# Performance work log

Measured on AMD Instinct MI355X. Metric: run time of the kernel, lower is better.

Reference implementation:

```python
import jax, jax.numpy as jnp
import numpy as np


def _conv2d(x, w, b=None):
    # 3x3, stride 1, pad 1, NCHW
    out = jax.lax.conv_general_dilated(x, w, (1, 1), ((1, 1), (1, 1)),
                                       dimension_numbers=('NCHW', 'OIHW', 'NCHW'))
    return out if b is None else out + b[None, :, None, None]


def _bn(x, g, beta, m, v, eps=1e-5):
    # inference-mode BatchNorm2d with running stats
    inv = g / jnp.sqrt(v + eps)
    return x * inv[None, :, None, None] + (beta - m * inv)[None, :, None, None]


def _se(x, w1, w2):
    # SELayer: global avgpool -> FC(C->C/r) -> ReLU -> FC(C/r->C) -> sigmoid -> scale
    s = x.mean((2, 3))                       # [B,C]
    s = jax.nn.sigmoid(jax.nn.relu(s @ w1.T) @ w2.T)
    return x * s[:, :, None, None]


def _bilinear(x, py, px):
    # zero-padded bilinear sampling; x [B,C,H,W], py/px [B,K,H,W] -> [B,C,K,H,W]
    B, C, H, W = x.shape
    K = py.shape[1]
    xf = x.reshape(B, C, H * W)
    y0 = jnp.floor(py)
    x0 = jnp.floor(px)
    out = jnp.zeros((B, C, K, H, W), x.dtype)
    for oy, ox in ((0., 0.), (0., 1.), (1., 0.), (1., 1.)):
        yc = y0 + oy
        xc = x0 + ox
        wgt = (1. - jnp.abs(py - yc)) * (1. - jnp.abs(px - xc))
        valid = ((yc >= 0) & (yc < H) & (xc >= 0) & (xc < W)).astype(x.dtype)
        idx = (jnp.clip(yc, 0, H - 1) * W + jnp.clip(xc, 0, W - 1)).astype(jnp.int32)
        g = jnp.take_along_axis(xf, idx.reshape(B, 1, -1), axis=2).reshape(B, C, K, H, W)
        out = out + g * (wgt * valid)[:, None]
    return out


def _dcnv2(x, w_off, b_off, w, b):
    # ModulatedDeformConv2dPack: conv_offset -> (o1,o2,mask); interleaved (dy,dx) pairs
    B, C, H, W = x.shape
    K = 9  # 3x3 kernel
    off = _conv2d(x, w_off, b_off)            # [B,27,H,W]
    o = off[:, :2 * K]
    mask = jax.nn.sigmoid(off[:, 2 * K:])     # [B,9,H,W]
    dy = o[:, 0::2]
    dx = o[:, 1::2]
    ky = (jnp.arange(K) // 3 - 1).astype(x.dtype)
    kx = (jnp.arange(K) % 3 - 1).astype(x.dtype)
    py = dy + jnp.arange(H, dtype=x.dtype)[None, None, :, None] + ky[None, :, None, None]
    px = dx + jnp.arange(W, dtype=x.dtype)[None, None, None, :] + kx[None, :, None, None]
    s = _bilinear(x, py, px) * mask[:, None]  # [B,C,9,H,W]
    return jnp.einsum('bckhw,ock->bohw', s, w.reshape(w.shape[0], C, K)) + b[None, :, None, None]


def _sfe(x, y, se_w1, se_w2, off_w, off_b, enc_w, enc_b,
         we_w, we_b, we_g, we_beta, we_m, we_v,
         wf_w, wf_b, wf_g, wf_beta, wf_m, wf_v):
    base = x + y
    base = base + _se(base, se_w1, se_w2)
    enc = jax.nn.relu(_dcnv2(base, off_w, off_b, enc_w, enc_b))
    w_e = jax.nn.sigmoid(_bn(_conv2d(enc, we_w, we_b), we_g, we_beta, we_m, we_v))
    w_f = jax.nn.sigmoid(_bn(_conv2d(enc, wf_w, wf_b), wf_g, wf_beta, wf_m, wf_v))
    return w_e * x + w_f * y


def setup_inputs() -> dict:
    B, C, CC, H, W = 4, 256, 64, 64, 64
    R = 16  # SE reduction
    key = jax.random.key(0)
    ks = jax.random.split(key, 12)
    f = jnp.float32
    return {
        'x': jax.random.normal(ks[0], (B, C, H, W), f),
        'y': jax.random.normal(ks[1], (B, C, H, W), f),
        'se_w1': jax.random.normal(ks[2], (C // R, C), f) * 0.05,
        'se_w2': jax.random.normal(ks[3], (C, C // R), f) * 0.05,
        'off_w': jax.random.normal(ks[4], (27, C, 3, 3), f) * 0.01,
        'off_b': jnp.zeros((27,), f),
        'enc_w': jax.random.normal(ks[5], (CC, C, 3, 3), f) * 0.02,
        'enc_b': jnp.zeros((CC,), f),
        'we_w': jax.random.normal(ks[6], (C, CC, 3, 3), f) * 0.02,
        'we_b': jnp.zeros((C,), f),
        'we_g': jnp.ones((C,), f),
        'we_beta': jnp.zeros((C,), f),
        'we_m': jax.random.normal(ks[7], (C,), f) * 0.01,
        'we_v': jnp.ones((C,), f),
        'wf_w': jax.random.normal(ks[8], (C, CC, 3, 3), f) * 0.02,
        'wf_b': jnp.zeros((C,), f),
        'wf_g': jnp.ones((C,), f),
        'wf_beta': jnp.zeros((C,), f),
        'wf_m': jax.random.normal(ks[9], (C,), f) * 0.01,
        'wf_v': jnp.ones((C,), f),
    }


def reference(x, y, se_w1, se_w2, off_w, off_b, enc_w, enc_b,
              we_w, we_b, we_g, we_beta, we_m, we_v,
              wf_w, wf_b, wf_g, wf_beta, wf_m, wf_v):
    return _sfe(x, y, se_w1, se_w2, off_w, off_b, enc_w, enc_b,
                we_w, we_b, we_g, we_beta, we_m, we_v,
                wf_w, wf_b, wf_g, wf_beta, wf_m, wf_v)
```

## Files before the change

### kernel.cpp

```cpp
#include <hip/hip_runtime.h>
#include <math.h>

#define BB 4
#define CH 256
#define CCH 64
#define HH 64
#define WW 64
#define HWN 4096

typedef short s8v __attribute__((ext_vector_type(8)));
typedef float f4v __attribute__((ext_vector_type(4)));

__device__ __forceinline__ float sigmoidf_(float v){ return 1.0f/(1.0f+__expf(-v)); }
__device__ __forceinline__ unsigned short f2bf(float f){
    union{float f; unsigned u;} v; v.f=f;
    unsigned r = v.u + 0x7FFF + ((v.u>>16)&1);
    return (unsigned short)(r>>16);
}
__device__ __forceinline__ float bf2f(unsigned short u){
    union{unsigned u; float f;} v; v.u = ((unsigned)u)<<16; return v.f;
}

__global__ __launch_bounds__(256) void k_prepall(const float* __restrict__ enc_w,
    const float* __restrict__ wew, const float* __restrict__ wfw, const float* __restrict__ ow,
    const float* __restrict__ web, const float* __restrict__ weg, const float* __restrict__ webt,
    const float* __restrict__ wem, const float* __restrict__ wev,
    const float* __restrict__ wfb, const float* __restrict__ wfg, const float* __restrict__ wfbt,
    const float* __restrict__ wfm, const float* __restrict__ wfv,
    unsigned short* __restrict__ wdcn, unsigned short* __restrict__ w2,
    unsigned short* __restrict__ wofft, float* __restrict__ bnp){
    int i = blockIdx.x*256+threadIdx.x;
    if (i < 147456){
        int oc = i/2304, kk = i-oc*2304;
        int k = kk>>8, c = kk&255;
        wdcn[i] = f2bf(enc_w[(size_t)oc*2304 + c*9 + k]);
        return;
    }
    int j = i - 147456;
    if (j < 294912){
        int row = j/576, k = j-row*576;
        int t = k>>6, ic = k&63;
        float v = (row<256)? wew[((row<<6)+ic)*9+t] : wfw[(((row-256)<<6)+ic)*9+t];
        w2[j] = f2bf(v);
        return;
    }
    int m = j - 294912;
    if (m < 73728){
        int ko = m/2304, k = m-ko*2304;
        int t = k>>8, c = k&255;
        wofft[m] = f2bf((ko<27)? ow[(size_t)(ko*256+c)*9+t] : 0.f);
        return;
    }
    int n = m - 73728;
    if (n < 256){
        float ie = weg[n]*rsqrtf(wev[n]+1e-5f);
        float se = webt[n]-wem[n]*ie+web[n]*ie;
        float iff = wfg[n]*rsqrtf(wfv[n]+1e-5f);
        float sf = wfbt[n]-wfm[n]*iff+wfb[n]*iff;
        *(float4*)(bnp+n*4) = make_float4(ie,se,iff,sf);
    }
}

__global__ __launch_bounds__(256) void k_base_sum(const float* __restrict__ x, const float* __restrict__ y,
                                                  float* __restrict__ base, float* __restrict__ sums){
    int bc = blockIdx.x, tid = threadIdx.x;
    const float* xp = x + (size_t)bc*HWN;
    const float* yp = y + (size_t)bc*HWN;
    float* bp = base + (size_t)bc*HWN;
    float s = 0.f;
    for (int i=tid;i<HWN;i+=256){ float v = xp[i]+yp[i]; bp[i]=v; s+=v; }
    __shared__ float red[256];
    red[tid]=s; __syncthreads();
    for (int off=128; off>0; off>>=1){ if (tid<off) red[tid]+=red[tid+off]; __syncthreads(); }
    if (tid==0) sums[bc]=red[0];
}

__global__ __launch_bounds__(256) void k_se(const float* __restrict__ sums, const float* __restrict__ w1,
                                            const float* __restrict__ w2, float* __restrict__ scale){
    int b = blockIdx.x, tid = threadIdx.x;
    __shared__ float sm[256];
    __shared__ float hid[16];
    sm[tid] = sums[b*256+tid]*(1.0f/4096.0f);
    __syncthreads();
    if (tid<16){
        float a=0.f; const float* wp = w1 + tid*256;
        for (int c=0;c<256;c++) a += sm[c]*wp[c];
        hid[tid]=fmaxf(a,0.f);
    }
    __syncthreads();
    float a=0.f; const float* wp = w2 + tid*16;
    #pragma unroll
    for (int j=0;j<16;j++) a += hid[j]*wp[j];
    scale[b*256+tid] = 1.f + sigmoidf_(a);
}

__global__ __launch_bounds__(256) void k_scale_t(const float* __restrict__ base, const float* __restrict__ scale,
                                                 unsigned short* __restrict__ base_t){
    int bid = blockIdx.x;
    int pb = bid&63, cb = (bid>>6)&3, b = bid>>8;
    int tid = threadIdx.x;
    __shared__ unsigned short lt[64*66];
    #pragma unroll
    for (int it=0; it<16; ++it){
        int idx = it*256 + tid;
        int c = idx>>6, p = idx&63;
        size_t gi = ((size_t)(b*256 + cb*64 + c))*4096 + pb*64 + p;
        float v = base[gi] * scale[b*256 + cb*64 + c];
        lt[p*66 + c] = f2bf(v);
    }
    __syncthreads();
    #pragma unroll
    for (int it=0; it<8; ++it){
        int idx = it*256 + tid;
        int p = idx>>5, cp = idx&31;
        unsigned lo = lt[p*66 + cp*2], hi = lt[p*66 + cp*2+1];
        *(unsigned*)(base_t + ((size_t)(b*4096 + pb*64 + p))*256 + cb*64 + cp*2) = lo | (hi<<16);
    }
}

__global__ __launch_bounds__(512) void k_offconv_mfma(const unsigned short* __restrict__ base_t,
    const unsigned short* __restrict__ wofft, const float* __restrict__ ob, float* __restrict__ off){
    int bid = blockIdx.x;
    int tIdx = bid&63, b = bid>>6;
    int th = tIdx>>3, tw = tIdx&7;
    int tid = threadIdx.x;
    __shared__ unsigned short plds[3200*8];
    const unsigned short* bt = base_t + (((size_t)b)<<12)*256;
    for (int i=tid; i<3200; i+=512){
        int spot = i>>5, cid = i&31;
        int sy = spot/10, sx = spot - sy*10;
        int gy = th*8 + sy - 1, gx = tw*8 + sx - 1;
        uint4 v = make_uint4(0u,0u,0u,0u);
        if (gy>=0 && gy<HH && gx>=0 && gx<WW)
            v = *(const uint4*)(bt + ((size_t)((gy<<6)+gx))*256 + cid*8);
        int chunk = (spot<<5) | (cid ^ (spot&7));
        *(uint4*)(plds + (chunk<<3)) = v;
    }
    __syncthreads();
    int lane = tid&63, w = tid>>6;
    int rf = w&1, pf = w>>1;
    int col = lane&15, kg = lane>>4;
    int p = pf*16 + col, ly = p>>3, lx = p&7;
    f4v acc = (f4v){0.f,0.f,0.f,0.f};
    #pragma unroll
    for (int j=0;j<9;j++){
        int dy = j/3, dx = j%3;
        int spot = (ly+dy)*10 + lx+dx;
        const unsigned short* arow = wofft + (size_t)(rf*16+col)*2304 + j*256 + kg*8;
        #pragma unroll
        for (int s=0;s<8;s++){
            s8v a = *(const s8v*)(arow + s*32);
            int cid = s*4 + kg;
            s8v bf = *(const s8v*)(plds + (((spot<<5)|(cid^(spot&7)))<<3));
            acc = __builtin_amdgcn_mfma_f32_16x16x32_bf16(a, bf, acc, 0,0,0);
        }
    }
    int gy = th*8+ly, gx = tw*8+lx;
    #pragma unroll
    for (int r=0;r<4;r++){
        int ko = rf*16 + kg*4 + r;
        if (ko < 27)
            off[(((size_t)(b*27+ko))<<12) + (gy<<6) + gx] = acc[r] + ob[ko];
    }
}

__global__ __launch_bounds__(256) void k_prep_off(const float* __restrict__ off,
                                                  float4* __restrict__ cwg, int4* __restrict__ cig){
    int i = blockIdx.x*256+threadIdx.x;
    if (i >= 147456) return;
    int b = i/36864, rem = i - b*36864;
    int k = rem>>12, pos = rem&4095;
    int h = pos>>6, p = pos&63;
    const float* op = off + ((size_t)b*27<<12) + pos;
    float dy = op[(size_t)(2*k)<<12];
    float dx = op[(size_t)(2*k+1)<<12];
    float m  = sigmoidf_(op[(size_t)(18+k)<<12]);
    float py = (float)(h + k/3 - 1) + dy;
    float px = (float)(p + (k%3) - 1) + dx;
    float y0 = floorf(py), x0 = floorf(px);
    float fy1 = py - y0, fy0 = 1.f - fy1;
    float fx1 = px - x0, fx0 = 1.f - fx1;
    int iy0 = (int)y0, ix0 = (int)x0;
    bool vy0 = (y0>=0.f)&&(y0<64.f), vy1 = (y0>=-1.f)&&(y0<63.f);
    bool vx0 = (x0>=0.f)&&(x0<64.f), vx1 = (x0>=-1.f)&&(x0<63.f);
    int cy0 = min(max(iy0,0),63), cy1 = min(max(iy0+1,0),63);
    int cx0 = min(max(ix0,0),63), cx1 = min(max(ix0+1,0),63);
    float4 wv; int4 iv;
    wv.x = (vy0&&vx0)? fy0*fx0*m : 0.f;
    wv.y = (vy0&&vx1)? fy0*fx1*m : 0.f;
    wv.z = (vy1&&vx0)? fy1*fx0*m : 0.f;
    wv.w = (vy1&&vx1)? fy1*fx1*m : 0.f;
    iv.x = cy0*WW+cx0; iv.y = cy0*WW+cx1; iv.z = cy1*WW+cx0; iv.w = cy1*WW+cx1;
    cwg[i] = wv; cig[i] = iv;
}

__global__ __launch_bounds__(512) void k_dcn_mfma(const unsigned short* __restrict__ base_t,
    const float4* __restrict__ cwg, const int4* __restrict__ cig,
    const unsigned short* __restrict__ wdcn, unsigned short* __restrict__ part2b){
    int bid = blockIdx.x;
    int cg = bid&3, b = (bid>>2)&3, h = bid>>4;
    int tid = threadIdx.x;
    __shared__ float4 cw4[576];
    __shared__ int4   ci4[576];
    __shared__ unsigned short smp[2][4096];

    for (int i=tid;i<576;i+=512){
        int k = i>>6, p = i&63;
        size_t g = (((size_t)b*9 + k)<<12) + (h<<6) + p;
        cw4[i] = cwg[g];
        ci4[i] = cig[g];
    }
    __syncthreads();

    int pos = tid>>3, cv = tid&7;
    int w = tid>>6, lane = tid&63;
    int mf = w&3, nh = w>>2;
    int col = lane&15, kg = lane>>4;
    f4v acc0 = (f4v){0.f,0.f,0.f,0.f}, acc1 = acc0;
    const unsigned short* bt = base_t + (((size_t)b)<<12)*256 + cg*64 + cv*8;
    const unsigned short* wrow = wdcn + (size_t)(mf*16+col)*2304 + cg*64;

    #pragma unroll
    for (int t=0;t<9;t++){
        float4 wv = cw4[t*64+pos];
        int4  iv = ci4[t*64+pos];
        uint4 r0 = *(const uint4*)(bt + ((size_t)iv.x<<8));
        uint4 r1 = *(const uint4*)(bt + ((size_t)iv.y<<8));
        uint4 r2 = *(const uint4*)(bt + ((size_t)iv.z<<8));
        uint4 r3 = *(const uint4*)(bt + ((size_t)iv.w<<8));
        const unsigned* q0=(const unsigned*)&r0;
        const unsigned* q1=(const unsigned*)&r1;
        const unsigned* q2=(const unsigned*)&r2;
        const unsigned* q3=(const unsigned*)&r3;
        unsigned pk[4];
        #pragma unroll
        for (int d=0;d<4;d++){
            float lo = wv.x*bf2f((unsigned short)(q0[d]&0xFFFFu)) + wv.y*bf2f((unsigned short)(q1[d]&0xFFFFu))
                     + wv.z*bf2f((unsigned short)(q2[d]&0xFFFFu)) + wv.w*bf2f((unsigned short)(q3[d]&0xFFFFu));
            float hi = wv.x*bf2f((unsigned short)(q0[d]>>16)) + wv.y*bf2f((unsigned short)(q1[d]>>16))
                     + wv.z*bf2f((unsigned short)(q2[d]>>16)) + wv.w*bf2f((unsigned short)(q3[d]>>16));
            pk[d] = (unsigned)f2bf(lo) | ((unsigned)f2bf(hi)<<16);
        }
        *(uint4*)(&smp[t&1][0] + (((pos<<3)|(cv^(pos&7)))<<3)) = *(const uint4*)pk;
        __syncthreads();
        const unsigned short* sb = &smp[t&1][0];
        #pragma unroll
        for (int ks=0;ks<2;ks++){
            s8v a = *(const s8v*)(wrow + t*256 + ks*32 + kg*8);
            int cgrp = ks*4+kg;
            int p0 = (nh*2)*16 + col;
            int p1 = p0 + 16;
            s8v b0 = *(const s8v*)(sb + (((p0<<3)|(cgrp^(p0&7)))<<3));
            s8v b1 = *(const s8v*)(sb + (((p1<<3)|(cgrp^(p1&7)))<<3));
            acc0 = __builtin_amdgcn_mfma_f32_16x16x32_bf16(a, b0, acc0, 0,0,0);
            acc1 = __builtin_amdgcn_mfma_f32_16x16x32_bf16(a, b1, acc1, 0,0,0);
        }
    }

    unsigned short* pout = part2b + ((size_t)(cg*BB + b))*(HWN*64);
    #pragma unroll
    for (int j=0;j<2;j++){
        f4v a = j ? acc1 : acc0;
        int posg = (h<<6) + (nh*2+j)*16 + col;
        int oc = mf*16 + kg*4;
        unsigned lo = (unsigned)f2bf(a[0]) | ((unsigned)f2bf(a[1])<<16);
        unsigned hi = (unsigned)f2bf(a[2]) | ((unsigned)f2bf(a[3])<<16);
        *(uint2*)(pout + (size_t)posg*64 + oc) = make_uint2(lo,hi);
    }
}

__global__ __launch_bounds__(256) void k_encreduce(const unsigned short* __restrict__ part2b,
                                                   const float* __restrict__ encb,
                                                   unsigned short* __restrict__ enc_t){
    int i = blockIdx.x*256+threadIdx.x;
    int b = i>>17, rem = i&131071;
    int pos = rem>>5, oc2 = rem&31;
    size_t basei = (((size_t)b<<12) + pos)*64 + oc2*2;
    float s0 = encb[oc2*2], s1 = encb[oc2*2+1];
    #pragma unroll
    for (int cg=0;cg<4;cg++){
        unsigned pv = *(const unsigned*)(part2b + (size_t)cg*1048576 + basei);
        s0 += bf2f((unsigned short)(pv & 0xFFFFu));
        s1 += bf2f((unsigned short)(pv >> 16));
    }
    unsigned short lo = f2bf(fmaxf(s0,0.f));
    unsigned short hi = f2bf(fmaxf(s1,0.f));
    *(unsigned int*)(enc_t + basei) = (unsigned int)lo | ((unsigned int)hi<<16);
}

__global__ __launch_bounds__(512) void k_fuse_mfma(const unsigned short* __restrict__ enc_t,
    const unsigned short* __restrict__ w2, const float* __restrict__ bnp,
    const float* __restrict__ x, const float* __restrict__ y, float* __restrict__ out){
    int bid = blockIdx.x;
    int ocg = bid&3, tile = (bid>>2)&15, b = bid>>6;
    int h0 = (tile>>2)<<4, w0 = (tile&3)<<4;
    int tid = threadIdx.x;
    __shared__ unsigned short elds[324*64];

    const unsigned short* ebase = enc_t + (((size_t)b)<<12)*64;
    #pragma unroll
    for (int kk=0;kk<6;kk++){
        int i = tid + kk*512;
        if (i < 2592){
            int sp = i>>3, icg = i&7;
            int sy = sp/18, sx = sp - sy*18;
            int py = h0+sy-1, px = w0+sx-1;
            uint4 v = make_uint4(0u,0u,0u,0u);
            if (py>=0 && py<HH && px>=0 && px<WW)
                v = *(const uint4*)(ebase + (size_t)((py<<6)+px)*64 + (icg<<3));
            int chunk = ((sp<<3) | icg) ^ (sp&7);
            *(uint4*)(elds + (chunk<<3)) = v;
        }
    }
    __syncthreads();

    int lane = tid&63, w = tid>>6;
    int col = lane&15, kg = lane>>4;
    f4v acc[8][2];
    #pragma unroll
    for (int rf=0;rf<8;rf++)
        #pragma unroll
        for (int pf=0;pf<2;pf++) acc[rf][pf] = (f4v){0.f,0.f,0.f,0.f};

    #pragma unroll
    for (int t=0;t<18;t++){
        const int j = t>>1, ih = t&1;
        const int dy = j/3-1, dx = j%3-1;
        s8v af[8];
        #pragma unroll
        for (int rf=0;rf<8;rf++){
            int row = (rf<4 ? ocg*64 + rf*16 : 256 + ocg*64 + (rf-4)*16) + col;
            af[rf] = *(const s8v*)(w2 + (size_t)row*576 + t*32 + kg*8);
        }
        s8v bfr[2];
        #pragma unroll
        for (int pf=0;pf<2;pf++){
            int tyc = w*2+pf;
            int sp = (tyc+dy+1)*18 + (col+dx+1);
            int chunk = ((sp<<3) | (ih*4+kg)) ^ (sp&7);
            bfr[pf] = *(const s8v*)(elds + (chunk<<3));
        }
        #pragma unroll
        for (int rf=0;rf<8;rf++)
            #pragma unroll
            for (int pf=0;pf<2;pf++)
                acc[rf][pf] = __builtin_amdgcn_mfma_f32_16x16x32_bf16(af[rf], bfr[pf], acc[rf][pf], 0,0,0);
    }

    #pragma unroll
    for (int rf=0;rf<4;rf++){
        #pragma unroll
        for (int pf=0;pf<2;pf++){
            int tyc = w*2+pf;
            int py = h0+tyc, px = w0+col;
            #pragma unroll
            for (int r=0;r<4;r++){
                int oc = ocg*64 + rf*16 + kg*4 + r;
                float4 bn = *(const float4*)(bnp + oc*4);
                float ve = sigmoidf_(acc[rf  ][pf][r]*bn.x + bn.y);
                float vf = sigmoidf_(acc[rf+4][pf][r]*bn.z + bn.w);
                size_t oi = (((size_t)((b<<8)+oc))<<12) + (py<<6) + px;
                out[oi] = ve*x[oi] + vf*y[oi];
            }
        }
    }
}

extern "C" void kernel_launch(void* const* d_in, const int* in_sizes, int n_in,
                              void* d_out, int out_size, void* d_ws, size_t ws_size,
                              hipStream_t stream) {
    const float* x     = (const float*)d_in[0];
    const float* y     = (const float*)d_in[1];
    const float* se_w1 = (const float*)d_in[2];
    const float* se_w2 = (const float*)d_in[3];
    const float* off_w = (const float*)d_in[4];
    const float* off_b = (const float*)d_in[5];
    const float* enc_w = (const float*)d_in[6];
    const float* enc_b = (const float*)d_in[7];
    const float* we_w  = (const float*)d_in[8];
    const float* we_b  = (const float*)d_in[9];
    const float* we_g  = (const float*)d_in[10];
    const float* we_bt = (const float*)d_in[11];
    const float* we_m  = (const float*)d_in[12];
    const float* we_v  = (const float*)d_in[13];
    const float* wf_w  = (const float*)d_in[14];
    const float* wf_b  = (const float*)d_in[15];
    const float* wf_g  = (const float*)d_in[16];
    const float* wf_bt = (const float*)d_in[17];
    const float* wf_m  = (const float*)d_in[18];
    const float* wf_v  = (const float*)d_in[19];
    float* out = (float*)d_out;

    float* ws     = (float*)d_ws;
    float* base   = ws;
    float* off    = base + 4194304;
    float* encT_f = off  + 442368;
    float* sums   = encT_f + 524288;
    float* scale  = sums + 1024;
    float* wdcn_f = scale + 1024;
    float* w2f    = wdcn_f + 73728;
    float* bnp    = w2f  + 147456;
    float* wofft_f= bnp  + 1024;
    float* cw_f   = wofft_f + 36864;
    float* ci_f   = cw_f + 589824;
    unsigned short* enc_t = (unsigned short*)encT_f;
    unsigned short* wdcn  = (unsigned short*)wdcn_f;
    unsigned short* w2    = (unsigned short*)w2f;
    unsigned short* wofft = (unsigned short*)wofft_f;
    float4* cwg = (float4*)cw_f;
    int4*   cig = (int4*)ci_f;
    unsigned short* base_t = (unsigned short*)out;
    unsigned short* part2b = (unsigned short*)out + 4194304;

    k_prepall     <<<2018, 256, 0, stream>>>(enc_w, we_w, wf_w, off_w,
                                             we_b, we_g, we_bt, we_m, we_v,
                                             wf_b, wf_g, wf_bt, wf_m, wf_v,
                                             wdcn, w2, wofft, bnp);
    k_base_sum    <<<1024, 256, 0, stream>>>(x, y, base, sums);
    k_se          <<<4,    256, 0, stream>>>(sums, se_w1, se_w2, scale);
    k_scale_t     <<<1024, 256, 0, stream>>>(base, scale, base_t);
    k_offconv_mfma<<<256,  512, 0, stream>>>(base_t, wofft, off_b, off);
    k_prep_off    <<<576,  256, 0, stream>>>(off, cwg, cig);
    k_dcn_mfma    <<<1024, 512, 0, stream>>>(base_t, cwg, cig, wdcn, part2b);
    k_encreduce   <<<2048, 256, 0, stream>>>(part2b, enc_b, enc_t);
    k_fuse_mfma   <<<256,  512, 0, stream>>>(enc_t, w2, bnp, x, y, out);
}
```

Before: 240.6 us.

## Fold SE channel scale into per-batch conv weights and fuse base transpose

The SE per-channel scale is now folded into per-batch bf16 copies of the DCN and offset-conv weights, so the activation no longer needs a scale pass. The x+y sum, channel sums (via wave shuffles and atomics) and the bf16 transpose are merged into a single kernel, removing the fp32 base buffer round trip. The fuse kernel also doubles its block count, with half the output channels per block, to raise parallelism. In exchange, weights are replicated per batch, a memset and atomic adds are added, and rounding shifts because the scale is applied to weights instead of activations.

```diff
diff --git a/kernel.cpp b/kernel.cpp
--- a/kernel.cpp
+++ b/kernel.cpp
@@ -21,37 +21,22 @@
     union{unsigned u; float f;} v; v.u = ((unsigned)u)<<16; return v.f;
 }
 
-__global__ __launch_bounds__(256) void k_prepall(const float* __restrict__ enc_w,
-    const float* __restrict__ wew, const float* __restrict__ wfw, const float* __restrict__ ow,
+__global__ __launch_bounds__(256) void k_prepall(
+    const float* __restrict__ wew, const float* __restrict__ wfw,
     const float* __restrict__ web, const float* __restrict__ weg, const float* __restrict__ webt,
     const float* __restrict__ wem, const float* __restrict__ wev,
     const float* __restrict__ wfb, const float* __restrict__ wfg, const float* __restrict__ wfbt,
     const float* __restrict__ wfm, const float* __restrict__ wfv,
-    unsigned short* __restrict__ wdcn, unsigned short* __restrict__ w2,
-    unsigned short* __restrict__ wofft, float* __restrict__ bnp){
+    unsigned short* __restrict__ w2, float* __restrict__ bnp){
     int i = blockIdx.x*256+threadIdx.x;
-    if (i < 147456){
-        int oc = i/2304, kk = i-oc*2304;
-        int k = kk>>8, c = kk&255;
-        wdcn[i] = f2bf(enc_w[(size_t)oc*2304 + c*9 + k]);
-        return;
-    }
-    int j = i - 147456;
-    if (j < 294912){
-        int row = j/576, k = j-row*576;
+    if (i < 294912){
+        int row = i/576, k = i-row*576;
         int t = k>>6, ic = k&63;
         float v = (row<256)? wew[((row<<6)+ic)*9+t] : wfw[(((row-256)<<6)+ic)*9+t];
-        w2[j] = f2bf(v);
+        w2[i] = f2bf(v);
         return;
     }
-    int m = j - 294912;
-    if (m < 73728){
-        int ko = m/2304, k = m-ko*2304;
-        int t = k>>8, c = k&255;
-        wofft[m] = f2bf((ko<27)? ow[(size_t)(ko*256+c)*9+t] : 0.f);
-        return;
-    }
-    int n = m - 73728;
+    int n = i - 294912;
     if (n < 256){
         float ie = weg[n]*rsqrtf(wev[n]+1e-5f);
         float se = webt[n]-wem[n]*ie+web[n]*ie;
@@ -61,18 +46,32 @@
     }
 }
 
-__global__ __launch_bounds__(256) void k_base_sum(const float* __restrict__ x, const float* __restrict__ y,
-                                                  float* __restrict__ base, float* __restrict__ sums){
-    int bc = blockIdx.x, tid = threadIdx.x;
-    const float* xp = x + (size_t)bc*HWN;
-    const float* yp = y + (size_t)bc*HWN;
-    float* bp = base + (size_t)bc*HWN;
-    float s = 0.f;
-    for (int i=tid;i<HWN;i+=256){ float v = xp[i]+yp[i]; bp[i]=v; s+=v; }
-    __shared__ float red[256];
-    red[tid]=s; __syncthreads();
-    for (int off=128; off>0; off>>=1){ if (tid<off) red[tid]+=red[tid+off]; __syncthreads(); }
-    if (tid==0) sums[bc]=red[0];
+__global__ __launch_bounds__(256) void k_base_sum_t(const float* __restrict__ x, const float* __restrict__ y,
+                                                    unsigned short* __restrict__ base_t, float* __restrict__ sums){
+    int bid = blockIdx.x;
+    int pb = bid&63, cb = (bid>>6)&3, b = bid>>8;
+    int tid = threadIdx.x, lane = tid&63, w = tid>>6;
+    __shared__ unsigned short lt[64*66];
+    #pragma unroll
+    for (int it=0; it<16; ++it){
+        int c = it*4 + w;
+        int p = lane;
+        size_t gi = ((size_t)(b*256 + cb*64 + c))*4096 + pb*64 + p;
+        float v = x[gi] + y[gi];
+        lt[p*66 + c] = f2bf(v);
+        float s = v;
+        #pragma unroll
+        for (int off=32; off; off>>=1) s += __shfl_down(s, off, 64);
+        if (lane==0) atomicAdd(&sums[b*256 + cb*64 + c], s);
+    }
+    __syncthreads();
+    #pragma unroll
+    for (int it=0; it<8; ++it){
+        int idx = it*256 + tid;
+        int p = idx>>5, cp = idx&31;
+        unsigned lo = lt[p*66 + cp*2], hi = lt[p*66 + cp*2+1];
+        *(unsigned*)(base_t + ((size_t)(b*4096 + pb*64 + p))*256 + cb*64 + cp*2) = lo | (hi<<16);
+    }
 }
 
 __global__ __launch_bounds__(256) void k_se(const float* __restrict__ sums, const float* __restrict__ w1,
@@ -94,32 +93,28 @@
     scale[b*256+tid] = 1.f + sigmoidf_(a);
 }
 
-__global__ __launch_bounds__(256) void k_scale_t(const float* __restrict__ base, const float* __restrict__ scale,
-                                                 unsigned short* __restrict__ base_t){
-    int bid = blockIdx.x;
-    int pb = bid&63, cb = (bid>>6)&3, b = bid>>8;
-    int tid = threadIdx.x;
-    __shared__ unsigned short lt[64*66];
-    #pragma unroll
-    for (int it=0; it<16; ++it){
-        int idx = it*256 + tid;
-        int c = idx>>6, p = idx&63;
-        size_t gi = ((size_t)(b*256 + cb*64 + c))*4096 + pb*64 + p;
-        float v = base[gi] * scale[b*256 + cb*64 + c];
-        lt[p*66 + c] = f2bf(v);
-    }
-    __syncthreads();
-    #pragma unroll
-    for (int it=0; it<8; ++it){
-        int idx = it*256 + tid;
-        int p = idx>>5, cp = idx&31;
-        unsigned lo = lt[p*66 + cp*2], hi = lt[p*66 + cp*2+1];
-        *(unsigned*)(base_t + ((size_t)(b*4096 + pb*64 + p))*256 + cb*64 + cp*2) = lo | (hi<<16);
+__global__ __launch_bounds__(256) void k_wscale(const float* __restrict__ enc_w, const float* __restrict__ ow,
+                                                const float* __restrict__ scale,
+                                                unsigned short* __restrict__ wdcn_b,
+                                                unsigned short* __restrict__ wofft_b){
+    int i = blockIdx.x*256+threadIdx.x;
+    if (i < 589824){
+        int b = i/147456, r = i-b*147456;
+        int oc = r/2304, kk = r-oc*2304;
+        int k = kk>>8, c = kk&255;
+        wdcn_b[i] = f2bf(enc_w[(size_t)oc*2304 + c*9 + k] * scale[b*256+c]);
+    } else {
+        int j = i - 589824;
+        int b = j/73728, r = j-b*73728;
+        int ko = r/2304, kk = r-ko*2304;
+        int k = kk>>8, c = kk&255;
+        float v = (ko<27)? ow[(size_t)(ko*256+c)*9 + k] * scale[b*256+c] : 0.f;
+        wofft_b[j] = f2bf(v);
     }
 }
 
 __global__ __launch_bounds__(512) void k_offconv_mfma(const unsigned short* __restrict__ base_t,
-    const unsigned short* __restrict__ wofft, const float* __restrict__ ob, float* __restrict__ off){
+    const unsigned short* __restrict__ wofft_b, const float* __restrict__ ob, float* __restrict__ off){
     int bid = blockIdx.x;
     int tIdx = bid&63, b = bid>>6;
     int th = tIdx>>3, tw = tIdx&7;
@@ -142,11 +137,12 @@
     int col = lane&15, kg = lane>>4;
     int p = pf*16 + col, ly = p>>3, lx = p&7;
     f4v acc = (f4v){0.f,0.f,0.f,0.f};
+    const unsigned short* wb = wofft_b + (size_t)b*73728;
     #pragma unroll
     for (int j=0;j<9;j++){
         int dy = j/3, dx = j%3;
         int spot = (ly+dy)*10 + lx+dx;
-        const unsigned short* arow = wofft + (size_t)(rf*16+col)*2304 + j*256 + kg*8;
+        const unsigned short* arow = wb + (size_t)(rf*16+col)*2304 + j*256 + kg*8;
         #pragma unroll
         for (int s=0;s<8;s++){
             s8v a = *(const s8v*)(arow + s*32);
@@ -196,7 +192,7 @@
 
 __global__ __launch_bounds__(512) void k_dcn_mfma(const unsigned short* __restrict__ base_t,
     const float4* __restrict__ cwg, const int4* __restrict__ cig,
-    const unsigned short* __restrict__ wdcn, unsigned short* __restrict__ part2b){
+    const unsigned short* __restrict__ wdcn_b, unsigned short* __restrict__ part2b){
     int bid = blockIdx.x;
     int cg = bid&3, b = (bid>>2)&3, h = bid>>4;
     int tid = threadIdx.x;
@@ -218,7 +214,7 @@
     int col = lane&15, kg = lane>>4;
     f4v acc0 = (f4v){0.f,0.f,0.f,0.f}, acc1 = acc0;
     const unsigned short* bt = base_t + (((size_t)b)<<12)*256 + cg*64 + cv*8;
-    const unsigned short* wrow = wdcn + (size_t)(mf*16+col)*2304 + cg*64;
+    const unsigned short* wrow = wdcn_b + (size_t)b*147456 + (size_t)(mf*16+col)*2304 + cg*64;
 
     #pragma unroll
     for (int t=0;t<9;t++){
@@ -292,7 +288,7 @@
     const unsigned short* __restrict__ w2, const float* __restrict__ bnp,
     const float* __restrict__ x, const float* __restrict__ y, float* __restrict__ out){
     int bid = blockIdx.x;
-    int ocg = bid&3, tile = (bid>>2)&15, b = bid>>6;
+    int ocg = bid&7, tile = (bid>>3)&15, b = bid>>7;
     int h0 = (tile>>2)<<4, w0 = (tile&3)<<4;
     int tid = threadIdx.x;
     __shared__ unsigned short elds[324*64];
@@ -316,9 +312,9 @@
 
     int lane = tid&63, w = tid>>6;
     int col = lane&15, kg = lane>>4;
-    f4v acc[8][2];
-    #pragma unroll
-    for (int rf=0;rf<8;rf++)
+    f4v acc[4][2];
+    #pragma unroll
+    for (int rf=0;rf<4;rf++)
         #pragma unroll
         for (int pf=0;pf<2;pf++) acc[rf][pf] = (f4v){0.f,0.f,0.f,0.f};
 
@@ -326,10 +322,10 @@
     for (int t=0;t<18;t++){
         const int j = t>>1, ih = t&1;
         const int dy = j/3-1, dx = j%3-1;
-        s8v af[8];
-        #pragma unroll
-        for (int rf=0;rf<8;rf++){
-            int row = (rf<4 ? ocg*64 + rf*16 : 256 + ocg*64 + (rf-4)*16) + col;
+        s8v af[4];
+        #pragma unroll
+        for (int rf=0;rf<4;rf++){
+            int row = (rf<2 ? ocg*32 + rf*16 : 256 + ocg*32 + (rf-2)*16) + col;
             af[rf] = *(const s8v*)(w2 + (size_t)row*576 + t*32 + kg*8);
         }
         s8v bfr[2];
@@ -341,24 +337,24 @@
             bfr[pf] = *(const s8v*)(elds + (chunk<<3));
         }
         #pragma unroll
-        for (int rf=0;rf<8;rf++)
+        for (int rf=0;rf<4;rf++)
             #pragma unroll
             for (int pf=0;pf<2;pf++)
                 acc[rf][pf] = __builtin_amdgcn_mfma_f32_16x16x32_bf16(af[rf], bfr[pf], acc[rf][pf], 0,0,0);
     }
 
     #pragma unroll
-    for (int rf=0;rf<4;rf++){
+    for (int rf=0;rf<2;rf++){
         #pragma unroll
         for (int pf=0;pf<2;pf++){
             int tyc = w*2+pf;
             int py = h0+tyc, px = w0+col;
             #pragma unroll
             for (int r=0;r<4;r++){
-                int oc = ocg*64 + rf*16 + kg*4 + r;
+                int oc = ocg*32 + rf*16 + kg*4 + r;
                 float4 bn = *(const float4*)(bnp + oc*4);
                 float ve = sigmoidf_(acc[rf  ][pf][r]*bn.x + bn.y);
-                float vf = sigmoidf_(acc[rf+4][pf][r]*bn.z + bn.w);
+                float vf = sigmoidf_(acc[rf+2][pf][r]*bn.z + bn.w);
                 size_t oi = (((size_t)((b<<8)+oc))<<12) + (py<<6) + px;
                 out[oi] = ve*x[oi] + vf*y[oi];
             }
@@ -391,37 +387,36 @@
     const float* wf_v  = (const float*)d_in[19];
     float* out = (float*)d_out;
 
-    float* ws     = (float*)d_ws;
-    float* base   = ws;
-    float* off    = base + 4194304;
-    float* encT_f = off  + 442368;
-    float* sums   = encT_f + 524288;
-    float* scale  = sums + 1024;
-    float* wdcn_f = scale + 1024;
-    float* w2f    = wdcn_f + 73728;
-    float* bnp    = w2f  + 147456;
-    float* wofft_f= bnp  + 1024;
-    float* cw_f   = wofft_f + 36864;
-    float* ci_f   = cw_f + 589824;
-    unsigned short* enc_t = (unsigned short*)encT_f;
-    unsigned short* wdcn  = (unsigned short*)wdcn_f;
-    unsigned short* w2    = (unsigned short*)w2f;
-    unsigned short* wofft = (unsigned short*)wofft_f;
+    float* ws      = (float*)d_ws;
+    float* off     = ws;
+    float* encT_f  = off + 442368;
+    float* sums    = encT_f + 524288;
+    float* scale   = sums + 1024;
+    float* w2f     = scale + 1024;
+    float* bnp     = w2f + 147456;
+    float* wdcnb_f = bnp + 1024;
+    float* wofftb_f= wdcnb_f + 294912;
+    float* cw_f    = wofftb_f + 147456;
+    float* ci_f    = cw_f + 589824;
+    unsigned short* enc_t   = (unsigned short*)encT_f;
+    unsigned short* w2      = (unsigned short*)w2f;
+    unsigned short* wdcn_b  = (unsigned short*)wdcnb_f;
+    unsigned short* wofft_b = (unsigned short*)wofftb_f;
     float4* cwg = (float4*)cw_f;
     int4*   cig = (int4*)ci_f;
     unsigned short* base_t = (unsigned short*)out;
     unsigned short* part2b = (unsigned short*)out + 4194304;
 
-    k_prepall     <<<2018, 256, 0, stream>>>(enc_w, we_w, wf_w, off_w,
+    hipMemsetAsync(sums, 0, 1024*sizeof(float), stream);
+    k_prepall     <<<1153, 256, 0, stream>>>(we_w, wf_w,
                                              we_b, we_g, we_bt, we_m, we_v,
-                                             wf_b, wf_g, wf_bt, wf_m, wf_v,
-                                             wdcn, w2, wofft, bnp);
-    k_base_sum    <<<1024, 256, 0, stream>>>(x, y, base, sums);
+                                             wf_b, wf_g, wf_bt, wf_m, wf_v, w2, bnp);
+    k_base_sum_t  <<<1024, 256, 0, stream>>>(x, y, base_t, sums);
     k_se          <<<4,    256, 0, stream>>>(sums, se_w1, se_w2, scale);
-    k_scale_t     <<<1024, 256, 0, stream>>>(base, scale, base_t);
-    k_offconv_mfma<<<256,  512, 0, stream>>>(base_t, wofft, off_b, off);
+    k_wscale      <<<3456, 256, 0, stream>>>(enc_w, off_w, scale, wdcn_b, wofft_b);
+    k_offconv_mfma<<<256,  512, 0, stream>>>(base_t, wofft_b, off_b, off);
     k_prep_off    <<<576,  256, 0, stream>>>(off, cwg, cig);
-    k_dcn_mfma    <<<1024, 512, 0, stream>>>(base_t, cwg, cig, wdcn, part2b);
+    k_dcn_mfma    <<<1024, 512, 0, stream>>>(base_t, cwg, cig, wdcn_b, part2b);
     k_encreduce   <<<2048, 256, 0, stream>>>(part2b, enc_b, enc_t);
-    k_fuse_mfma   <<<256,  512, 0, stream>>>(enc_t, w2, bnp, x, y, out);
-}
+    k_fuse_mfma   <<<512,  512, 0, stream>>>(enc_t, w2, bnp, x, y, out);
+}
```

Result: slower. 259.7 us (+7.9%).

## Retile fuse conv kernel into smaller 8x8 spatial tiles with more blocks

Applied to the files above, without the earlier changes.

The final fused conv+BN+sigmoid+blend kernel now runs 2048 blocks of 256 threads over 8x8 spatial tiles with 32 output channels per block, instead of 256 blocks of 512 threads over 16x16 tiles with 64 channels. The goal is to fill far more of the GPU's compute units and cut per-thread accumulator registers, since the old 256-block grid left many CUs idle. In exchange, the 10x10 halo costs proportionally more redundant enc_t loads, B fragments are reused across fewer MFMAs, and weight rows are re-read by more blocks.

```diff
diff --git a/kernel.cpp b/kernel.cpp
--- a/kernel.cpp
+++ b/kernel.cpp
@@ -288,80 +288,61 @@
     *(unsigned int*)(enc_t + basei) = (unsigned int)lo | ((unsigned int)hi<<16);
 }
 
-__global__ __launch_bounds__(512) void k_fuse_mfma(const unsigned short* __restrict__ enc_t,
+__global__ __launch_bounds__(256) void k_fuse_mfma(const unsigned short* __restrict__ enc_t,
     const unsigned short* __restrict__ w2, const float* __restrict__ bnp,
     const float* __restrict__ x, const float* __restrict__ y, float* __restrict__ out){
     int bid = blockIdx.x;
-    int ocg = bid&3, tile = (bid>>2)&15, b = bid>>6;
-    int h0 = (tile>>2)<<4, w0 = (tile&3)<<4;
+    int ocg = bid&7, tIdx = (bid>>3)&63, b = bid>>9;
+    int th = tIdx>>3, tw = tIdx&7;
     int tid = threadIdx.x;
-    __shared__ unsigned short elds[324*64];
+    __shared__ unsigned short elds[6400];
 
     const unsigned short* ebase = enc_t + (((size_t)b)<<12)*64;
-    #pragma unroll
-    for (int kk=0;kk<6;kk++){
-        int i = tid + kk*512;
-        if (i < 2592){
-            int sp = i>>3, icg = i&7;
-            int sy = sp/18, sx = sp - sy*18;
-            int py = h0+sy-1, px = w0+sx-1;
-            uint4 v = make_uint4(0u,0u,0u,0u);
-            if (py>=0 && py<HH && px>=0 && px<WW)
-                v = *(const uint4*)(ebase + (size_t)((py<<6)+px)*64 + (icg<<3));
-            int chunk = ((sp<<3) | icg) ^ (sp&7);
-            *(uint4*)(elds + (chunk<<3)) = v;
-        }
+    for (int i=tid; i<800; i+=256){
+        int spot = i>>3, icg = i&7;
+        int sy = spot/10, sx = spot - sy*10;
+        int gy = th*8 + sy - 1, gx = tw*8 + sx - 1;
+        uint4 v = make_uint4(0u,0u,0u,0u);
+        if (gy>=0 && gy<HH && gx>=0 && gx<WW)
+            v = *(const uint4*)(ebase + (size_t)((gy<<6)+gx)*64 + (icg<<3));
+        int chunk = (spot<<3) | (icg ^ (spot&7));
+        *(uint4*)(elds + (chunk<<3)) = v;
     }
     __syncthreads();
 
     int lane = tid&63, w = tid>>6;
     int col = lane&15, kg = lane>>4;
-    f4v acc[8][2];
-    #pragma unroll
-    for (int rf=0;rf<8;rf++)
-        #pragma unroll
-        for (int pf=0;pf<2;pf++) acc[rf][pf] = (f4v){0.f,0.f,0.f,0.f};
+    int p = w*16 + col, ly = p>>3, lx = p&7;
+    f4v acc[4];
+    #pragma unroll
+    for (int rf=0;rf<4;rf++) acc[rf] = (f4v){0.f,0.f,0.f,0.f};
 
     #pragma unroll
     for (int t=0;t<18;t++){
         const int j = t>>1, ih = t&1;
-        const int dy = j/3-1, dx = j%3-1;
-        s8v af[8];
+        const int dy = j/3, dx = j%3;
+        int spot = (ly+dy)*10 + lx+dx;
+        int cgrp = ih*4+kg;
+        s8v bfr = *(const s8v*)(elds + (((spot<<3)|(cgrp^(spot&7)))<<3));
         #pragma unroll
-        for (int rf=0;rf<8;rf++){
-            int row = (rf<4 ? ocg*64 + rf*16 : 256 + ocg*64 + (rf-4)*16) + col;
-            af[rf] = *(const s8v*)(w2 + (size_t)row*576 + t*32 + kg*8);
+        for (int rf=0;rf<4;rf++){
+            int row = (rf<2 ? ocg*32 + rf*16 : 256 + ocg*32 + (rf-2)*16) + col;
+            s8v a = *(const s8v*)(w2 + (size_t)row*576 + t*32 + kg*8);
+            acc[rf] = __builtin_amdgcn_mfma_f32_16x16x32_bf16(a, bfr, acc[rf], 0,0,0);
         }
-        s8v bfr[2];
+    }
+
+    int gy = th*8+ly, gx = tw*8+lx;
+    #pragma unroll
+    for (int rf=0;rf<2;rf++){
         #pragma unroll
-        for (int pf=0;pf<2;pf++){
-            int tyc = w*2+pf;
-            int sp = (tyc+dy+1)*18 + (col+dx+1);
-            int chunk = ((sp<<3) | (ih*4+kg)) ^ (sp&7);
-            bfr[pf] = *(const s8v*)(elds + (chunk<<3));
-        }
-        #pragma unroll
-        for (int rf=0;rf<8;rf++)
-            #pragma unroll
-            for (int pf=0;pf<2;pf++)
-                acc[rf][pf] = __builtin_amdgcn_mfma_f32_16x16x32_bf16(af[rf], bfr[pf], acc[rf][pf], 0,0,0);
-    }
-
-    #pragma unroll
-    for (int rf=0;rf<4;rf++){
-        #pragma unroll
-        for (int pf=0;pf<2;pf++){
-            int tyc = w*2+pf;
-            int py = h0+tyc, px = w0+col;
-            #pragma unroll
-            for (int r=0;r<4;r++){
-                int oc = ocg*64 + rf*16 + kg*4 + r;
-                float4 bn = *(const float4*)(bnp + oc*4);
-                float ve = sigmoidf_(acc[rf  ][pf][r]*bn.x + bn.y);
-                float vf = sigmoidf_(acc[rf+4][pf][r]*bn.z + bn.w);
-                size_t oi = (((size_t)((b<<8)+oc))<<12) + (py<<6) + px;
-                out[oi] = ve*x[oi] + vf*y[oi];
-            }
+        for (int r=0;r<4;r++){
+            int oc = ocg*32 + rf*16 + kg*4 + r;
+            float4 bn = *(const float4*)(bnp + oc*4);
+            float ve = sigmoidf_(acc[rf  ][r]*bn.x + bn.y);
+            float vf = sigmoidf_(acc[rf+2][r]*bn.z + bn.w);
+            size_t oi = (((size_t)((b<<8)+oc))<<12) + (gy<<6) + gx;
+            out[oi] = ve*x[oi] + vf*y[oi];
         }
     }
 }
@@ -423,5 +404,5 @@
     k_prep_off    <<<576,  256, 0, stream>>>(off, cwg, cig);
     k_dcn_mfma    <<<1024, 512, 0, stream>>>(base_t, cwg, cig, wdcn, part2b);
     k_encreduce   <<<2048, 256, 0, stream>>>(part2b, enc_b, enc_t);
-    k_fuse_mfma   <<<256,  512, 0, stream>>>(enc_t, w2, bnp, x, y, out);
-}
+    k_fuse_mfma   <<<2048, 256, 0, stream>>>(enc_t, w2, bnp, x, y, out);
+}
```

Result: slower. 259.5 us (+7.9%).
